# Kernel optimization log

Hardware: AMD Instinct MI355X
Metric: run time of the kernel (lower is better)

The kernel has to match this reference:

```python
import jax, jax.numpy as jnp
import numpy as np

D_MODEL = 64

def setup_inputs() -> dict:
    key = jax.random.key(0)
    k1, k2, k3, k4 = jax.random.split(key, 4)
    B, T, E = 4, 4096, 128
    x = jax.random.normal(k1, (B, T, E), dtype=jnp.float32)
    # nn.Linear weights, stored transposed as (in, out) for x @ W
    s = 1.0 / np.sqrt(E)
    Wq = jax.random.uniform(k2, (E, D_MODEL), jnp.float32, -s, s)
    Wk = jax.random.uniform(k3, (E, D_MODEL), jnp.float32, -s, s)
    Wv = jax.random.uniform(k4, (E, D_MODEL), jnp.float32, -s, s)
    return {"x": x, "Wq": Wq, "Wk": Wk, "Wv": Wv}

def reference(x, Wq, Wk, Wv):
    B, T, E = x.shape
    q = jnp.einsum('bte,ed->btd', x, Wq)
    k = jnp.einsum('bte,ed->btd', x, Wk)
    v = jnp.einsum('bte,ed->btd', x, Wv)
    scores = jnp.einsum('bqd,bkd->bqk', q, k) / np.sqrt(D_MODEL)  # [B,T,T]
    causal = jnp.tril(jnp.ones((T, T), dtype=bool))
    scores = jnp.where(causal, scores, jnp.float32(-1e9))
    attn = jax.nn.softmax(scores, axis=-1)
    # dropout p=0.0 -> identity (eval-mode faithful)
    return jnp.einsum('bqk,bkd->bqd', attn, v)
```

## Files before the change

kernel.cpp:

```cpp
#include <hip/hip_runtime.h>
#include <hip/hip_bf16.h>


typedef __attribute__((ext_vector_type(4))) float  f32x4;
typedef __attribute__((ext_vector_type(4))) unsigned int u32x4;
typedef __attribute__((ext_vector_type(8))) __bf16 bf16x8;
typedef __attribute__((ext_vector_type(8))) unsigned short u16x8;
typedef __attribute__((ext_vector_type(4))) unsigned short u16x4;

#define T_SEQ 4096
#define DH    64
#define EDIM  128
#define KVB   64
#define KSTR  72

__device__ __forceinline__ unsigned short f2bf(float f) {
    unsigned int x = __builtin_bit_cast(unsigned int, f);
    unsigned int r = x + 0x7fffu + ((x >> 16) & 1u);
    return (unsigned short)(r >> 16);
}

__device__ __forceinline__ unsigned int cvt_pk_bf16(float lo, float hi) {
    unsigned int d;
    asm("v_cvt_pk_bf16_f32 %0, %1, %2" : "=v"(d) : "v"(lo), "v"(hi));
    return d;
}

__device__ __forceinline__ f32x4 mfma_bf16(u16x8 a, u16x8 b, f32x4 c) {
    return __builtin_amdgcn_mfma_f32_16x16x32_bf16(
        __builtin_bit_cast(bf16x8, a), __builtin_bit_cast(bf16x8, b), c, 0, 0, 0);
}

__global__ __launch_bounds__(256) void prep_w_kernel(
    const float* __restrict__ wq, const float* __restrict__ wk,
    const float* __restrict__ wv, unsigned short* __restrict__ wt)
{
    int o = blockIdx.x * 256 + threadIdx.x;
    int m   = o >> 13;
    int rem = o & 8191;
    int d = rem >> 7, e = rem & 127;
    const float* W = (m == 0) ? wq : (m == 1) ? wk : wv;
    wt[o] = f2bf(W[e * DH + d]);
}

__global__ __launch_bounds__(64) void proj_kernel(
    const float* __restrict__ x, const unsigned short* __restrict__ wt,
    unsigned short* __restrict__ qw, unsigned short* __restrict__ kw,
    unsigned short* __restrict__ vt)
{
    const int l   = threadIdx.x;
    const int l15 = l & 15;
    const int lg  = l >> 4;
    const int row0 = blockIdx.x * 16;
    const int b    = row0 >> 12;
    const int t0   = row0 & 4095;

    u16x8 af[4];
    #pragma unroll
    for (int kt = 0; kt < 4; ++kt) {
        const float* xp = x + (row0 + l15) * EDIM + kt * 32 + lg * 8;
        f32x4 a = *(const f32x4*)xp;
        f32x4 bb = *(const f32x4*)(xp + 4);
        af[kt] = u16x8{ f2bf(a[0]), f2bf(a[1]), f2bf(a[2]), f2bf(a[3]),
                        f2bf(bb[0]), f2bf(bb[1]), f2bf(bb[2]), f2bf(bb[3]) };
    }

    unsigned short* outs[2] = { qw, kw };
    #pragma unroll
    for (int m = 0; m < 2; ++m) {
        #pragma unroll
        for (int nt = 0; nt < 4; ++nt) {
            f32x4 acc = {};
            #pragma unroll
            for (int kt = 0; kt < 4; ++kt) {
                u16x8 bfrag = *(const u16x8*)(wt + (m * 64 + nt * 16 + l15) * EDIM
                                                 + kt * 32 + lg * 8);
                acc = mfma_bf16(af[kt], bfrag, acc);
            }
            const float sc = (m == 0) ? 0.125f : 1.0f;
            #pragma unroll
            for (int r = 0; r < 4; ++r)
                outs[m][(row0 + lg * 4 + r) * DH + nt * 16 + l15] = f2bf(acc[r] * sc);
        }
    }

    #pragma unroll
    for (int nt = 0; nt < 4; ++nt) {
        f32x4 acc = {};
        #pragma unroll
        for (int kt = 0; kt < 4; ++kt) {
            u16x8 bfrag = *(const u16x8*)(wt + (2 * 64 + nt * 16 + l15) * EDIM
                                             + kt * 32 + lg * 8);
            acc = mfma_bf16(af[kt], bfrag, acc);
        }
        u16x4 pv = { f2bf(acc[0]), f2bf(acc[1]), f2bf(acc[2]), f2bf(acc[3]) };
        *(u16x4*)(vt + ((size_t)(b * DH + nt * 16 + l15)) * T_SEQ + t0 + lg * 4) = pv;
    }
}

struct St32s {
    f32x4 o[2][4];
    float m[2], l[2];
};

__device__ __forceinline__ void load_qf(
    const unsigned short* __restrict__ qg, int base, int qrow0,
    int l15, int lg, u16x8 qf[2][2])
{
    #pragma unroll
    for (int rt = 0; rt < 2; ++rt) {
        const unsigned short* qrow = qg + (base + qrow0 + rt * 16 + l15) * DH;
        qf[rt][0] = *(const u16x8*)(qrow + 0 + lg * 8);
        qf[rt][1] = *(const u16x8*)(qrow + 32 + lg * 8);
    }
}

__global__ __launch_bounds__(256, 4) void attn_partial_kernel(
    const unsigned short* __restrict__ qg, const unsigned short* __restrict__ kg,
    const unsigned short* __restrict__ vt,
    unsigned short* __restrict__ po, float* __restrict__ pm, float* __restrict__ pl)
{
    const int bid  = blockIdx.x;
    const int ch   = bid & 15;
    const int q128 = (bid >> 4) & 31;
    const int b    = bid >> 9;
    if (2 * ch > q128) return;

    __shared__ unsigned short K_lds[64 * KSTR];
    __shared__ unsigned short V_lds[64 * KSTR];

    const int tid = threadIdx.x;
    const int w   = tid >> 6;
    const int l   = tid & 63;
    const int l15 = l & 15;
    const int lg  = l >> 4;

    const int base   = b * T_SEQ;
    const int qrow0w = q128 * 128 + w * 32;
    const int kvb = ch * 256;
    const int kve = min(kvb + 256, q128 * 128 + 128);

    u16x8 qf[2][2];
    load_qf(qg, base, qrow0w, l15, lg, qf);

    St32s st;
    #pragma unroll
    for (int rt = 0; rt < 2; ++rt) {
        #pragma unroll
        for (int dt = 0; dt < 4; ++dt) st.o[rt][dt] = f32x4{};
        st.m[rt] = -1e30f; st.l[rt] = 0.0f;
    }

    const int src0 = l15 + 32 * (lg & 1);
    const int src1 = src0 + 16;
    const bool hi  = (lg >> 1) != 0;

    for (int kv0 = kvb; kv0 < kve; kv0 += KVB) {
        #pragma unroll
        for (int i = 0; i < 2; ++i) {
            int idx = tid + i * 256;
            int row = idx >> 3;
            int c8  = (idx & 7) * 8;
            *(u16x8*)&K_lds[row * KSTR + c8] =
                *(const u16x8*)(kg + (size_t)(base + kv0 + row) * DH + c8);
            *(u16x8*)&V_lds[row * KSTR + c8] =
                *(const u16x8*)(vt + (size_t)(b * DH + row) * T_SEQ + kv0 + c8);
        }
        __syncthreads();

        if (kv0 <= qrow0w + 31) {
            u16x8 kf[4][2];
            #pragma unroll
            for (int nt = 0; nt < 4; ++nt)
                #pragma unroll
                for (int kt = 0; kt < 2; ++kt)
                    kf[nt][kt] = *(const u16x8*)&K_lds[(nt * 16 + l15) * KSTR
                                                       + kt * 32 + lg * 8];

            f32x4 s[2][4];
            __builtin_amdgcn_s_setprio(1);
            #pragma unroll
            for (int rt = 0; rt < 2; ++rt)
                #pragma unroll
                for (int nt = 0; nt < 4; ++nt) {
                    f32x4 a = {};
                    a = mfma_bf16(kf[nt][0], qf[rt][0], a);
                    a = mfma_bf16(kf[nt][1], qf[rt][1], a);
                    s[rt][nt] = a;
                }
            __builtin_amdgcn_s_setprio(0);

            if (kv0 + KVB - 1 > qrow0w) {
                #pragma unroll
                for (int rt = 0; rt < 2; ++rt)
                    #pragma unroll
                    for (int nt = 0; nt < 4; ++nt)
                        #pragma unroll
                        for (int r = 0; r < 4; ++r) {
                            int kj = kv0 + nt * 16 + lg * 4 + r;
                            int qi = qrow0w + rt * 16 + l15;
                            if (kj > qi) s[rt][nt][r] = -1e30f;
                        }
            }

            float sc2[2];
            bool grow = false;
            unsigned int pk[2][4][2];
            #pragma unroll
            for (int rt = 0; rt < 2; ++rt) {
                float mx = s[rt][0][0];
                #pragma unroll
                for (int nt = 0; nt < 4; ++nt)
                    #pragma unroll
                    for (int r = 0; r < 4; ++r)
                        mx = fmaxf(mx, s[rt][nt][r]);
                mx = fmaxf(mx, __shfl_xor(mx, 16));
                mx = fmaxf(mx, __shfl_xor(mx, 32));

                float mold = st.m[rt];
                float mnew = fmaxf(mold, mx);
                grow |= (mx > mold);
                float sc = __expf(mold - mnew);
                sc2[rt] = sc;
                st.m[rt] = mnew;

                float rs = 0.0f;
                #pragma unroll
                for (int nt = 0; nt < 4; ++nt)
                    #pragma unroll
                    for (int r = 0; r < 4; ++r) {
                        float p = __expf(s[rt][nt][r] - mnew);
                        s[rt][nt][r] = p;
                        rs += p;
                    }
                rs += __shfl_xor(rs, 16);
                rs += __shfl_xor(rs, 32);
                st.l[rt] = st.l[rt] * sc + rs;

                #pragma unroll
                for (int nt = 0; nt < 4; ++nt) {
                    pk[rt][nt][0] = cvt_pk_bf16(s[rt][nt][0], s[rt][nt][1]);
                    pk[rt][nt][1] = cvt_pk_bf16(s[rt][nt][2], s[rt][nt][3]);
                }
            }
            if (__any(grow)) {
                #pragma unroll
                for (int rt = 0; rt < 2; ++rt)
                    #pragma unroll
                    for (int dt = 0; dt < 4; ++dt)
                        st.o[rt][dt] *= sc2[rt];
            }

            __builtin_amdgcn_s_setprio(1);
            #pragma unroll
            for (int kt = 0; kt < 2; ++kt) {
                u16x8 vf[4];
                #pragma unroll
                for (int dt = 0; dt < 4; ++dt)
                    vf[dt] = *(const u16x8*)&V_lds[(dt * 16 + l15) * KSTR
                                                   + kt * 32 + lg * 8];
                #pragma unroll
                for (int rt = 0; rt < 2; ++rt) {
                    unsigned int pb[4];
                    #pragma unroll
                    for (int t = 0; t < 4; ++t) {
                        int src = (t < 2) ? src0 : src1;
                        unsigned int pa  = __shfl(pk[rt][2 * kt][t & 1], src);
                        unsigned int pbv = __shfl(pk[rt][2 * kt + 1][t & 1], src);
                        pb[t] = hi ? pbv : pa;
                    }
                    u32x4 pbq = { pb[0], pb[1], pb[2], pb[3] };
                    u16x8 pbf = __builtin_bit_cast(u16x8, pbq);
                    #pragma unroll
                    for (int dt = 0; dt < 4; ++dt)
                        st.o[rt][dt] = mfma_bf16(vf[dt], pbf, st.o[rt][dt]);
                }
            }
            __builtin_amdgcn_s_setprio(0);
        }
        __syncthreads();
    }

    const int pidx = (b * 32 + q128) * 16 + ch;
    unsigned short* pob = po + (size_t)pidx * 8192;
    #pragma unroll
    for (int rt = 0; rt < 2; ++rt) {
        int row = w * 32 + rt * 16 + l15;
        #pragma unroll
        for (int dt = 0; dt < 4; ++dt) {
            unsigned int w0 = cvt_pk_bf16(st.o[rt][dt][0], st.o[rt][dt][1]);
            unsigned int w1 = cvt_pk_bf16(st.o[rt][dt][2], st.o[rt][dt][3]);
            *(unsigned int*)&pob[row * 64 + dt * 16 + lg * 4]     = w0;
            *(unsigned int*)&pob[row * 64 + dt * 16 + lg * 4 + 2] = w1;
        }
        if (lg == 0) {
            pm[pidx * 128 + row] = st.m[rt];
            pl[pidx * 128 + row] = st.l[rt];
        }
    }
}

__global__ __launch_bounds__(256) void attn_combine_kernel(
    const unsigned short* __restrict__ po, const float* __restrict__ pm,
    const float* __restrict__ pl, float* __restrict__ out)
{
    const int blk  = blockIdx.x;
    const int half = blk & 1;
    const int tb   = blk >> 1;
    const int q128 = tb & 31;
    const int b    = tb >> 5;
    const int nch  = (q128 >> 1) + 1;
    const int row  = half * 64 + (threadIdx.x >> 2);
    const int d0   = (threadIdx.x & 3) * 16;
    const int bp   = tb * 16;

    float mstar = -1e30f;
    for (int i = 0; i < nch; ++i)
        mstar = fmaxf(mstar, pm[(bp + i) * 128 + row]);

    float lsum = 0.0f;
    float a[16] = {};
    for (int i = 0; i < nch; ++i) {
        float wi = __expf(pm[(bp + i) * 128 + row] - mstar);
        lsum += wi * pl[(bp + i) * 128 + row];
        const unsigned short* p = po + (size_t)(bp + i) * 8192 + row * 64 + d0;
        u16x8 v0 = *(const u16x8*)p;
        u16x8 v1 = *(const u16x8*)(p + 8);
        #pragma unroll
        for (int j = 0; j < 8; ++j) {
            unsigned int u0 = (unsigned int)v0[j] << 16;
            unsigned int u1 = (unsigned int)v1[j] << 16;
            a[j]     += wi * __builtin_bit_cast(float, u0);
            a[8 + j] += wi * __builtin_bit_cast(float, u1);
        }
    }
    const float inv = 1.0f / lsum;
    float* op = out + (size_t)(b * T_SEQ + q128 * 128 + row) * DH + d0;
    #pragma unroll
    for (int j = 0; j < 4; ++j) {
        f32x4 o0 = { a[4*(j&1)+0 + 8*(j>>1)] * inv, a[4*(j&1)+1 + 8*(j>>1)] * inv,
                     a[4*(j&1)+2 + 8*(j>>1)] * inv, a[4*(j&1)+3 + 8*(j>>1)] * inv };
        *(f32x4*)(op + j * 4) = o0;
    }
}

__device__ __forceinline__ void flash32s_global(
    const unsigned short* __restrict__ kp,
    const unsigned short* __restrict__ vp,
    int qrow0, int kv_begin, int kv_end,
    const u16x8 qf[2][2], St32s& st, int l15, int lg)
{
    const int src0 = l15 + 32 * (lg & 1);
    const int src1 = src0 + 16;
    const bool hi  = (lg >> 1) != 0;

    for (int kv0 = kv_begin; kv0 < kv_end; kv0 += KVB) {
        u16x8 kf[4][2];
        #pragma unroll
        for (int nt = 0; nt < 4; ++nt)
            #pragma unroll
            for (int kt = 0; kt < 2; ++kt)
                kf[nt][kt] = *(const u16x8*)(kp + (kv0 + nt * 16 + l15) * DH
                                                + kt * 32 + lg * 8);

        f32x4 s[2][4];
        #pragma unroll
        for (int rt = 0; rt < 2; ++rt)
            #pragma unroll
            for (int nt = 0; nt < 4; ++nt) {
                f32x4 a = {};
                a = mfma_bf16(kf[nt][0], qf[rt][0], a);
                a = mfma_bf16(kf[nt][1], qf[rt][1], a);
                s[rt][nt] = a;
            }

        if (kv0 + KVB - 1 > qrow0) {
            #pragma unroll
            for (int rt = 0; rt < 2; ++rt)
                #pragma unroll
                for (int nt = 0; nt < 4; ++nt)
                    #pragma unroll
                    for (int r = 0; r < 4; ++r) {
                        int kj = kv0 + nt * 16 + lg * 4 + r;
                        int qi = qrow0 + rt * 16 + l15;
                        if (kj > qi) s[rt][nt][r] = -1e30f;
                    }
        }

        float sc2[2];
        bool grow = false;
        unsigned int pk[2][4][2];
        #pragma unroll
        for (int rt = 0; rt < 2; ++rt) {
            float mx = s[rt][0][0];
            #pragma unroll
            for (int nt = 0; nt < 4; ++nt)
                #pragma unroll
                for (int r = 0; r < 4; ++r)
                    mx = fmaxf(mx, s[rt][nt][r]);
            mx = fmaxf(mx, __shfl_xor(mx, 16));
            mx = fmaxf(mx, __shfl_xor(mx, 32));

            float mold = st.m[rt];
            float mnew = fmaxf(mold, mx);
            grow |= (mx > mold);
            float sc = __expf(mold - mnew);
            sc2[rt] = sc;
            st.m[rt] = mnew;

            float rs = 0.0f;
            #pragma unroll
            for (int nt = 0; nt < 4; ++nt)
                #pragma unroll
                for (int r = 0; r < 4; ++r) {
                    float p = __expf(s[rt][nt][r] - mnew);
                    s[rt][nt][r] = p;
                    rs += p;
                }
            rs += __shfl_xor(rs, 16);
            rs += __shfl_xor(rs, 32);
            st.l[rt] = st.l[rt] * sc + rs;

            #pragma unroll
            for (int nt = 0; nt < 4; ++nt) {
                pk[rt][nt][0] = cvt_pk_bf16(s[rt][nt][0], s[rt][nt][1]);
                pk[rt][nt][1] = cvt_pk_bf16(s[rt][nt][2], s[rt][nt][3]);
            }
        }
        if (__any(grow)) {
            #pragma unroll
            for (int rt = 0; rt < 2; ++rt)
                #pragma unroll
                for (int dt = 0; dt < 4; ++dt)
                    st.o[rt][dt] *= sc2[rt];
        }

        #pragma unroll
        for (int kt = 0; kt < 2; ++kt) {
            u16x8 vf[4];
            #pragma unroll
            for (int dt = 0; dt < 4; ++dt)
                vf[dt] = *(const u16x8*)(vp + (size_t)(dt * 16 + l15) * T_SEQ
                                            + kv0 + kt * 32 + lg * 8);
            #pragma unroll
            for (int rt = 0; rt < 2; ++rt) {
                unsigned int pb[4];
                #pragma unroll
                for (int t = 0; t < 4; ++t) {
                    int src = (t < 2) ? src0 : src1;
                    unsigned int pa  = __shfl(pk[rt][2 * kt][t & 1], src);
                    unsigned int pbv = __shfl(pk[rt][2 * kt + 1][t & 1], src);
                    pb[t] = hi ? pbv : pa;
                }
                u32x4 pbq = { pb[0], pb[1], pb[2], pb[3] };
                u16x8 pbf = __builtin_bit_cast(u16x8, pbq);
                #pragma unroll
                for (int dt = 0; dt < 4; ++dt)
                    st.o[rt][dt] = mfma_bf16(vf[dt], pbf, st.o[rt][dt]);
            }
        }
    }
}

__global__ __launch_bounds__(64, 4) void attn_direct_kernel(
    const unsigned short* __restrict__ qg, const unsigned short* __restrict__ kg,
    const unsigned short* __restrict__ vt, float* __restrict__ out)
{
    const int bid = blockIdx.x;
    const int q32 = bid & 127;
    const int b   = bid >> 7;
    const int l = threadIdx.x, l15 = l & 15, lg = l >> 4;
    const int qrow0 = q32 * 32;
    const int base  = b * T_SEQ;

    u16x8 qf[2][2];
    load_qf(qg, base, qrow0, l15, lg, qf);

    St32s st;
    #pragma unroll
    for (int rt = 0; rt < 2; ++rt) {
        #pragma unroll
        for (int dt = 0; dt < 4; ++dt) st.o[rt][dt] = f32x4{};
        st.m[rt] = -1e30f; st.l[rt] = 0.0f;
    }

    flash32s_global(kg + (size_t)base * DH, vt + (size_t)b * DH * T_SEQ,
                    qrow0, 0, qrow0 + 32, qf, st, l15, lg);

    #pragma unroll
    for (int rt = 0; rt < 2; ++rt) {
        float inv = 1.0f / st.l[rt];
        int row = base + qrow0 + rt * 16 + l15;
        #pragma unroll
        for (int dt = 0; dt < 4; ++dt) {
            f32x4 ov = st.o[rt][dt] * inv;
            *(f32x4*)&out[(size_t)row * DH + dt * 16 + lg * 4] = ov;
        }
    }
}

extern "C" void kernel_launch(void* const* d_in, const int* in_sizes, int n_in,
                              void* d_out, int out_size, void* d_ws, size_t ws_size,
                              hipStream_t stream)
{
    const float* x  = (const float*)d_in[0];
    const float* wq = (const float*)d_in[1];
    const float* wk = (const float*)d_in[2];
    const float* wv = (const float*)d_in[3];
    float* out = (float*)d_out;

    unsigned short* wt = (unsigned short*)d_ws;
    unsigned short* qw = (unsigned short*)((char*)d_ws + 65536);
    unsigned short* kw = qw + (size_t)16384 * DH;
    unsigned short* vt = kw + (size_t)16384 * DH;

    const size_t po_off = 65536u + 3u * 16384u * DH * 2u;
    const size_t po_sz  = (size_t)2048 * 128 * 64 * 2;
    const size_t pm_off = po_off + po_sz;
    const size_t pl_off = pm_off + (size_t)2048 * 128 * 4;
    const size_t need   = pl_off + (size_t)2048 * 128 * 4;

    prep_w_kernel<<<96, 256, 0, stream>>>(wq, wk, wv, wt);
    proj_kernel<<<1024, 64, 0, stream>>>(x, wt, qw, kw, vt);

    if (ws_size >= need) {
        unsigned short* po = (unsigned short*)((char*)d_ws + po_off);
        float* pm = (float*)((char*)d_ws + pm_off);
        float* pl = (float*)((char*)d_ws + pl_off);
        attn_partial_kernel<<<4 * 32 * 16, 256, 0, stream>>>(qw, kw, vt, po, pm, pl);
        attn_combine_kernel<<<4 * 32 * 2, 256, 0, stream>>>(po, pm, pl, out);
    } else {
        attn_direct_kernel<<<4 * 128, 64, 0, stream>>>(qw, kw, vt, out);
    }
}
```

Measured before the change: 69.90 us.

## Compact causal grid, prefetch second KV half into registers, use exp2 softmax

Replaces the 16-chunk grid that early-exits masked blocks with a compact triangular mapping of 272 live blocks per batch, decoded via sqrt. Each block stages 128 keys of K/V into larger LDS buffers at once and register-prefetches the second 128 while computing the first, cutting per-tile barriers and hiding global latency. Q is prescaled by log2(e)/8 so softmax and combine use exp2f instead of __expf. Larger LDS lowers the occupancy hint from 4 to 3 blocks, and more registers are held live for the prefetch.

After: 60.53 us. -13.4%, faster.

```diff
diff --git a/kernel.cpp b/kernel.cpp
--- a/kernel.cpp
+++ b/kernel.cpp
@@ -13,6 +13,8 @@
 #define EDIM  128
 #define KVB   64
 #define KSTR  72
+#define VSTR  136
+#define QSCALE 0.18033688f
 
 __device__ __forceinline__ unsigned short f2bf(float f) {
     unsigned int x = __builtin_bit_cast(unsigned int, f);
@@ -77,7 +79,7 @@
                                                  + kt * 32 + lg * 8);
                 acc = mfma_bf16(af[kt], bfrag, acc);
             }
-            const float sc = (m == 0) ? 0.125f : 1.0f;
+            const float sc = (m == 0) ? QSCALE : 1.0f;
             #pragma unroll
             for (int r = 0; r < 4; ++r)
                 outs[m][(row0 + lg * 4 + r) * DH + nt * 16 + l15] = f2bf(acc[r] * sc);
@@ -98,36 +100,57 @@
     }
 }
 
-struct St32s {
-    f32x4 o[2][4];
-    float m[2], l[2];
-};
-
-__device__ __forceinline__ void load_qf(
-    const unsigned short* __restrict__ qg, int base, int qrow0,
-    int l15, int lg, u16x8 qf[2][2])
-{
-    #pragma unroll
-    for (int rt = 0; rt < 2; ++rt) {
-        const unsigned short* qrow = qg + (base + qrow0 + rt * 16 + l15) * DH;
-        qf[rt][0] = *(const u16x8*)(qrow + 0 + lg * 8);
-        qf[rt][1] = *(const u16x8*)(qrow + 32 + lg * 8);
-    }
-}
-
-__global__ __launch_bounds__(256, 4) void attn_partial_kernel(
+__device__ __forceinline__ void loadK(u16x8 kr[4], const unsigned short* kgB,
+                                      int kv0, int tid) {
+    #pragma unroll
+    for (int j = 0; j < 4; ++j) {
+        int gi = tid + j * 256;
+        kr[j] = *(const u16x8*)(kgB + (size_t)(kv0 + (gi >> 3)) * DH + (gi & 7) * 8);
+    }
+}
+__device__ __forceinline__ void loadV(u16x8 vr[4], const unsigned short* vtB,
+                                      int kv0, int tid) {
+    #pragma unroll
+    for (int j = 0; j < 4; ++j) {
+        int gi = tid + j * 256;
+        vr[j] = *(const u16x8*)(vtB + (size_t)(gi >> 4) * T_SEQ + kv0 + (gi & 15) * 8);
+    }
+}
+__device__ __forceinline__ void writeK(const u16x8 kr[4], unsigned short* K_lds,
+                                       int tid) {
+    #pragma unroll
+    for (int j = 0; j < 4; ++j) {
+        int gi = tid + j * 256;
+        *(u16x8*)&K_lds[(gi >> 3) * KSTR + (gi & 7) * 8] = kr[j];
+    }
+}
+__device__ __forceinline__ void writeV(const u16x8 vr[4], unsigned short* V_lds,
+                                       int tid) {
+    #pragma unroll
+    for (int j = 0; j < 4; ++j) {
+        int gi = tid + j * 256;
+        *(u16x8*)&V_lds[(gi >> 4) * VSTR + (gi & 15) * 8] = vr[j];
+    }
+}
+
+__global__ __launch_bounds__(256, 3) void attn_partial_kernel(
     const unsigned short* __restrict__ qg, const unsigned short* __restrict__ kg,
     const unsigned short* __restrict__ vt,
     unsigned short* __restrict__ po, float* __restrict__ pm, float* __restrict__ pl)
 {
-    const int bid  = blockIdx.x;
-    const int ch   = bid & 15;
-    const int q128 = (bid >> 4) & 31;
-    const int b    = bid >> 9;
-    if (2 * ch > q128) return;
-
-    __shared__ unsigned short K_lds[64 * KSTR];
-    __shared__ unsigned short V_lds[64 * KSTR];
+    const int bid = blockIdx.x;
+    const int b   = bid / 272;
+    const int i   = bid - b * 272;
+    int k = (int)((__builtin_sqrtf((float)(4 * i + 1)) - 1.0f) * 0.5f);
+    while (k * (k + 1) > i) --k;
+    while ((k + 1) * (k + 2) <= i) ++k;
+    const int r    = i - k * (k + 1);
+    const int hiq  = (r >= k + 1);
+    const int q128 = 2 * k + hiq;
+    const int ch   = hiq ? r - (k + 1) : r;
+
+    __shared__ unsigned short K_lds[128 * KSTR];
+    __shared__ unsigned short V_lds[64 * VSTR];
 
     const int tid = threadIdx.x;
     const int w   = tid >> 6;
@@ -139,146 +162,166 @@
     const int qrow0w = q128 * 128 + w * 32;
     const int kvb = ch * 256;
     const int kve = min(kvb + 256, q128 * 128 + 128);
+    const bool ng2 = (kve - kvb) > 128;
+
+    const unsigned short* kgB = kg + (size_t)base * DH;
+    const unsigned short* vtB = vt + (size_t)b * DH * T_SEQ;
 
     u16x8 qf[2][2];
-    load_qf(qg, base, qrow0w, l15, lg, qf);
-
-    St32s st;
     #pragma unroll
     for (int rt = 0; rt < 2; ++rt) {
-        #pragma unroll
-        for (int dt = 0; dt < 4; ++dt) st.o[rt][dt] = f32x4{};
-        st.m[rt] = -1e30f; st.l[rt] = 0.0f;
+        const unsigned short* qrow = qg + (base + qrow0w + rt * 16 + l15) * DH;
+        qf[rt][0] = *(const u16x8*)(qrow + 0 + lg * 8);
+        qf[rt][1] = *(const u16x8*)(qrow + 32 + lg * 8);
+    }
+
+    f32x4 o_acc[2][4];
+    float m_run[2], l_run[2];
+    #pragma unroll
+    for (int rt = 0; rt < 2; ++rt) {
+        #pragma unroll
+        for (int dt = 0; dt < 4; ++dt) o_acc[rt][dt] = f32x4{};
+        m_run[rt] = -1e30f; l_run[rt] = 0.0f;
     }
 
     const int src0 = l15 + 32 * (lg & 1);
     const int src1 = src0 + 16;
     const bool hi  = (lg >> 1) != 0;
 
-    for (int kv0 = kvb; kv0 < kve; kv0 += KVB) {
-        #pragma unroll
-        for (int i = 0; i < 2; ++i) {
-            int idx = tid + i * 256;
-            int row = idx >> 3;
-            int c8  = (idx & 7) * 8;
-            *(u16x8*)&K_lds[row * KSTR + c8] =
-                *(const u16x8*)(kg + (size_t)(base + kv0 + row) * DH + c8);
-            *(u16x8*)&V_lds[row * KSTR + c8] =
-                *(const u16x8*)(vt + (size_t)(b * DH + row) * T_SEQ + kv0 + c8);
-        }
-        __syncthreads();
-
-        if (kv0 <= qrow0w + 31) {
-            u16x8 kf[4][2];
-            #pragma unroll
-            for (int nt = 0; nt < 4; ++nt)
-                #pragma unroll
-                for (int kt = 0; kt < 2; ++kt)
-                    kf[nt][kt] = *(const u16x8*)&K_lds[(nt * 16 + l15) * KSTR
-                                                       + kt * 32 + lg * 8];
-
-            f32x4 s[2][4];
-            __builtin_amdgcn_s_setprio(1);
+    auto compute_tile = [&](int kv0, int tt) {
+        if (kv0 > qrow0w + 31) return;
+        const unsigned short* Kt = K_lds + (tt * 64) * KSTR;
+        const unsigned short* Vt = V_lds + tt * 64;
+
+        u16x8 kf[4][2];
+        #pragma unroll
+        for (int nt = 0; nt < 4; ++nt)
+            #pragma unroll
+            for (int kt = 0; kt < 2; ++kt)
+                kf[nt][kt] = *(const u16x8*)&Kt[(nt * 16 + l15) * KSTR
+                                                + kt * 32 + lg * 8];
+
+        f32x4 s[2][4];
+        __builtin_amdgcn_s_setprio(1);
+        #pragma unroll
+        for (int rt = 0; rt < 2; ++rt)
+            #pragma unroll
+            for (int nt = 0; nt < 4; ++nt) {
+                f32x4 a = {};
+                a = mfma_bf16(kf[nt][0], qf[rt][0], a);
+                a = mfma_bf16(kf[nt][1], qf[rt][1], a);
+                s[rt][nt] = a;
+            }
+        __builtin_amdgcn_s_setprio(0);
+
+        if (kv0 + KVB - 1 > qrow0w) {
             #pragma unroll
             for (int rt = 0; rt < 2; ++rt)
-                #pragma unroll
-                for (int nt = 0; nt < 4; ++nt) {
-                    f32x4 a = {};
-                    a = mfma_bf16(kf[nt][0], qf[rt][0], a);
-                    a = mfma_bf16(kf[nt][1], qf[rt][1], a);
-                    s[rt][nt] = a;
-                }
-            __builtin_amdgcn_s_setprio(0);
-
-            if (kv0 + KVB - 1 > qrow0w) {
-                #pragma unroll
-                for (int rt = 0; rt < 2; ++rt)
-                    #pragma unroll
-                    for (int nt = 0; nt < 4; ++nt)
-                        #pragma unroll
-                        for (int r = 0; r < 4; ++r) {
-                            int kj = kv0 + nt * 16 + lg * 4 + r;
-                            int qi = qrow0w + rt * 16 + l15;
-                            if (kj > qi) s[rt][nt][r] = -1e30f;
-                        }
-            }
-
-            float sc2[2];
-            bool grow = false;
-            unsigned int pk[2][4][2];
-            #pragma unroll
-            for (int rt = 0; rt < 2; ++rt) {
-                float mx = s[rt][0][0];
                 #pragma unroll
                 for (int nt = 0; nt < 4; ++nt)
                     #pragma unroll
-                    for (int r = 0; r < 4; ++r)
-                        mx = fmaxf(mx, s[rt][nt][r]);
-                mx = fmaxf(mx, __shfl_xor(mx, 16));
-                mx = fmaxf(mx, __shfl_xor(mx, 32));
-
-                float mold = st.m[rt];
-                float mnew = fmaxf(mold, mx);
-                grow |= (mx > mold);
-                float sc = __expf(mold - mnew);
-                sc2[rt] = sc;
-                st.m[rt] = mnew;
-
-                float rs = 0.0f;
-                #pragma unroll
-                for (int nt = 0; nt < 4; ++nt)
-                    #pragma unroll
-                    for (int r = 0; r < 4; ++r) {
-                        float p = __expf(s[rt][nt][r] - mnew);
-                        s[rt][nt][r] = p;
-                        rs += p;
+                    for (int rr = 0; rr < 4; ++rr) {
+                        int kj = kv0 + nt * 16 + lg * 4 + rr;
+                        int qi = qrow0w + rt * 16 + l15;
+                        if (kj > qi) s[rt][nt][rr] = -1e30f;
                     }
-                rs += __shfl_xor(rs, 16);
-                rs += __shfl_xor(rs, 32);
-                st.l[rt] = st.l[rt] * sc + rs;
-
-                #pragma unroll
-                for (int nt = 0; nt < 4; ++nt) {
-                    pk[rt][nt][0] = cvt_pk_bf16(s[rt][nt][0], s[rt][nt][1]);
-                    pk[rt][nt][1] = cvt_pk_bf16(s[rt][nt][2], s[rt][nt][3]);
+        }
+
+        float sc2[2];
+        bool grow = false;
+        unsigned int pk[2][4][2];
+        #pragma unroll
+        for (int rt = 0; rt < 2; ++rt) {
+            float mx = s[rt][0][0];
+            #pragma unroll
+            for (int nt = 0; nt < 4; ++nt)
+                #pragma unroll
+                for (int rr = 0; rr < 4; ++rr)
+                    mx = fmaxf(mx, s[rt][nt][rr]);
+            mx = fmaxf(mx, __shfl_xor(mx, 16));
+            mx = fmaxf(mx, __shfl_xor(mx, 32));
+
+            float mold = m_run[rt];
+            float mnew = fmaxf(mold, mx);
+            grow |= (mx > mold);
+            float sc = exp2f(mold - mnew);
+            sc2[rt] = sc;
+            m_run[rt] = mnew;
+
+            float rs = 0.0f;
+            #pragma unroll
+            for (int nt = 0; nt < 4; ++nt)
+                #pragma unroll
+                for (int rr = 0; rr < 4; ++rr) {
+                    float p = exp2f(s[rt][nt][rr] - mnew);
+                    s[rt][nt][rr] = p;
+                    rs += p;
                 }
-            }
-            if (__any(grow)) {
-                #pragma unroll
-                for (int rt = 0; rt < 2; ++rt)
-                    #pragma unroll
-                    for (int dt = 0; dt < 4; ++dt)
-                        st.o[rt][dt] *= sc2[rt];
-            }
-
-            __builtin_amdgcn_s_setprio(1);
-            #pragma unroll
-            for (int kt = 0; kt < 2; ++kt) {
-                u16x8 vf[4];
+            rs += __shfl_xor(rs, 16);
+            rs += __shfl_xor(rs, 32);
+            l_run[rt] = l_run[rt] * sc + rs;
+
+            #pragma unroll
+            for (int nt = 0; nt < 4; ++nt) {
+                pk[rt][nt][0] = cvt_pk_bf16(s[rt][nt][0], s[rt][nt][1]);
+                pk[rt][nt][1] = cvt_pk_bf16(s[rt][nt][2], s[rt][nt][3]);
+            }
+        }
+        if (__any(grow)) {
+            #pragma unroll
+            for (int rt = 0; rt < 2; ++rt)
                 #pragma unroll
                 for (int dt = 0; dt < 4; ++dt)
-                    vf[dt] = *(const u16x8*)&V_lds[(dt * 16 + l15) * KSTR
-                                                   + kt * 32 + lg * 8];
-                #pragma unroll
-                for (int rt = 0; rt < 2; ++rt) {
-                    unsigned int pb[4];
-                    #pragma unroll
-                    for (int t = 0; t < 4; ++t) {
-                        int src = (t < 2) ? src0 : src1;
-                        unsigned int pa  = __shfl(pk[rt][2 * kt][t & 1], src);
-                        unsigned int pbv = __shfl(pk[rt][2 * kt + 1][t & 1], src);
-                        pb[t] = hi ? pbv : pa;
-                    }
-                    u32x4 pbq = { pb[0], pb[1], pb[2], pb[3] };
-                    u16x8 pbf = __builtin_bit_cast(u16x8, pbq);
-                    #pragma unroll
-                    for (int dt = 0; dt < 4; ++dt)
-                        st.o[rt][dt] = mfma_bf16(vf[dt], pbf, st.o[rt][dt]);
+                    o_acc[rt][dt] *= sc2[rt];
+        }
+
+        __builtin_amdgcn_s_setprio(1);
+        #pragma unroll
+        for (int kt = 0; kt < 2; ++kt) {
+            u16x8 vf[4];
+            #pragma unroll
+            for (int dt = 0; dt < 4; ++dt)
+                vf[dt] = *(const u16x8*)&Vt[(dt * 16 + l15) * VSTR
+                                            + kt * 32 + lg * 8];
+            #pragma unroll
+            for (int rt = 0; rt < 2; ++rt) {
+                unsigned int pb[4];
+                #pragma unroll
+                for (int t = 0; t < 4; ++t) {
+                    int src = (t < 2) ? src0 : src1;
+                    unsigned int pa  = __shfl(pk[rt][2 * kt][t & 1], src);
+                    unsigned int pbv = __shfl(pk[rt][2 * kt + 1][t & 1], src);
+                    pb[t] = hi ? pbv : pa;
                 }
-            }
-            __builtin_amdgcn_s_setprio(0);
-        }
+                u32x4 pbq = { pb[0], pb[1], pb[2], pb[3] };
+                u16x8 pbf = __builtin_bit_cast(u16x8, pbq);
+                #pragma unroll
+                for (int dt = 0; dt < 4; ++dt)
+                    o_acc[rt][dt] = mfma_bf16(vf[dt], pbf, o_acc[rt][dt]);
+            }
+        }
+        __builtin_amdgcn_s_setprio(0);
+    };
+
+    u16x8 kr[4], vr[4];
+    loadK(kr, kgB, kvb, tid);
+    loadV(vr, vtB, kvb, tid);
+    writeK(kr, K_lds, tid);
+    writeV(vr, V_lds, tid);
+    __syncthreads();
+
+    if (ng2) loadK(kr, kgB, kvb + 128, tid);
+    compute_tile(kvb, 0);
+    if (ng2) loadV(vr, vtB, kvb + 128, tid);
+    compute_tile(kvb + 64, 1);
+    __syncthreads();
+
+    if (ng2) {
+        writeK(kr, K_lds, tid);
+        writeV(vr, V_lds, tid);
         __syncthreads();
+        compute_tile(kvb + 128, 0);
+        compute_tile(kvb + 192, 1);
     }
 
     const int pidx = (b * 32 + q128) * 16 + ch;
@@ -288,14 +331,14 @@
         int row = w * 32 + rt * 16 + l15;
         #pragma unroll
         for (int dt = 0; dt < 4; ++dt) {
-            unsigned int w0 = cvt_pk_bf16(st.o[rt][dt][0], st.o[rt][dt][1]);
-            unsigned int w1 = cvt_pk_bf16(st.o[rt][dt][2], st.o[rt][dt][3]);
+            unsigned int w0 = cvt_pk_bf16(o_acc[rt][dt][0], o_acc[rt][dt][1]);
+            unsigned int w1 = cvt_pk_bf16(o_acc[rt][dt][2], o_acc[rt][dt][3]);
             *(unsigned int*)&pob[row * 64 + dt * 16 + lg * 4]     = w0;
             *(unsigned int*)&pob[row * 64 + dt * 16 + lg * 4 + 2] = w1;
         }
         if (lg == 0) {
-            pm[pidx * 128 + row] = st.m[rt];
-            pl[pidx * 128 + row] = st.l[rt];
+            pm[pidx * 128 + row] = m_run[rt];
+            pl[pidx * 128 + row] = l_run[rt];
         }
     }
 }
@@ -321,7 +364,7 @@
     float lsum = 0.0f;
     float a[16] = {};
     for (int i = 0; i < nch; ++i) {
-        float wi = __expf(pm[(bp + i) * 128 + row] - mstar);
+        float wi = exp2f(pm[(bp + i) * 128 + row] - mstar);
         lsum += wi * pl[(bp + i) * 128 + row];
         const unsigned short* p = po + (size_t)(bp + i) * 8192 + row * 64 + d0;
         u16x8 v0 = *(const u16x8*)p;
@@ -341,124 +384,6 @@
         f32x4 o0 = { a[4*(j&1)+0 + 8*(j>>1)] * inv, a[4*(j&1)+1 + 8*(j>>1)] * inv,
                      a[4*(j&1)+2 + 8*(j>>1)] * inv, a[4*(j&1)+3 + 8*(j>>1)] * inv };
         *(f32x4*)(op + j * 4) = o0;
-    }
-}
-
-__device__ __forceinline__ void flash32s_global(
-    const unsigned short* __restrict__ kp,
-    const unsigned short* __restrict__ vp,
-    int qrow0, int kv_begin, int kv_end,
-    const u16x8 qf[2][2], St32s& st, int l15, int lg)
-{
-    const int src0 = l15 + 32 * (lg & 1);
-    const int src1 = src0 + 16;
-    const bool hi  = (lg >> 1) != 0;
-
-    for (int kv0 = kv_begin; kv0 < kv_end; kv0 += KVB) {
-        u16x8 kf[4][2];
-        #pragma unroll
-        for (int nt = 0; nt < 4; ++nt)
-            #pragma unroll
-            for (int kt = 0; kt < 2; ++kt)
-                kf[nt][kt] = *(const u16x8*)(kp + (kv0 + nt * 16 + l15) * DH
-                                                + kt * 32 + lg * 8);
-
-        f32x4 s[2][4];
-        #pragma unroll
-        for (int rt = 0; rt < 2; ++rt)
-            #pragma unroll
-            for (int nt = 0; nt < 4; ++nt) {
-                f32x4 a = {};
-                a = mfma_bf16(kf[nt][0], qf[rt][0], a);
-                a = mfma_bf16(kf[nt][1], qf[rt][1], a);
-                s[rt][nt] = a;
-            }
-
-        if (kv0 + KVB - 1 > qrow0) {
-            #pragma unroll
-            for (int rt = 0; rt < 2; ++rt)
-                #pragma unroll
-                for (int nt = 0; nt < 4; ++nt)
-                    #pragma unroll
-                    for (int r = 0; r < 4; ++r) {
-                        int kj = kv0 + nt * 16 + lg * 4 + r;
-                        int qi = qrow0 + rt * 16 + l15;
-                        if (kj > qi) s[rt][nt][r] = -1e30f;
-                    }
-        }
-
-        float sc2[2];
-        bool grow = false;
-        unsigned int pk[2][4][2];
-        #pragma unroll
-        for (int rt = 0; rt < 2; ++rt) {
-            float mx = s[rt][0][0];
-            #pragma unroll
-            for (int nt = 0; nt < 4; ++nt)
-                #pragma unroll
-                for (int r = 0; r < 4; ++r)
-                    mx = fmaxf(mx, s[rt][nt][r]);
-            mx = fmaxf(mx, __shfl_xor(mx, 16));
-            mx = fmaxf(mx, __shfl_xor(mx, 32));
-
-            float mold = st.m[rt];
-            float mnew = fmaxf(mold, mx);
-            grow |= (mx > mold);
-            float sc = __expf(mold - mnew);
-            sc2[rt] = sc;
-            st.m[rt] = mnew;
-
-            float rs = 0.0f;
-            #pragma unroll
-            for (int nt = 0; nt < 4; ++nt)
-                #pragma unroll
-                for (int r = 0; r < 4; ++r) {
-                    float p = __expf(s[rt][nt][r] - mnew);
-                    s[rt][nt][r] = p;
-                    rs += p;
-                }
-            rs += __shfl_xor(rs, 16);
-            rs += __shfl_xor(rs, 32);
-            st.l[rt] = st.l[rt] * sc + rs;
-
-            #pragma unroll
-            for (int nt = 0; nt < 4; ++nt) {
-                pk[rt][nt][0] = cvt_pk_bf16(s[rt][nt][0], s[rt][nt][1]);
-                pk[rt][nt][1] = cvt_pk_bf16(s[rt][nt][2], s[rt][nt][3]);
-            }
-        }
-        if (__any(grow)) {
-            #pragma unroll
-            for (int rt = 0; rt < 2; ++rt)
-                #pragma unroll
-                for (int dt = 0; dt < 4; ++dt)
-                    st.o[rt][dt] *= sc2[rt];
-        }
-
-        #pragma unroll
-        for (int kt = 0; kt < 2; ++kt) {
-            u16x8 vf[4];
-            #pragma unroll
-            for (int dt = 0; dt < 4; ++dt)
-                vf[dt] = *(const u16x8*)(vp + (size_t)(dt * 16 + l15) * T_SEQ
-                                            + kv0 + kt * 32 + lg * 8);
-            #pragma unroll
-            for (int rt = 0; rt < 2; ++rt) {
-                unsigned int pb[4];
-                #pragma unroll
-                for (int t = 0; t < 4; ++t) {
-                    int src = (t < 2) ? src0 : src1;
-                    unsigned int pa  = __shfl(pk[rt][2 * kt][t & 1], src);
-                    unsigned int pbv = __shfl(pk[rt][2 * kt + 1][t & 1], src);
-                    pb[t] = hi ? pbv : pa;
-                }
-                u32x4 pbq = { pb[0], pb[1], pb[2], pb[3] };
-                u16x8 pbf = __builtin_bit_cast(u16x8, pbq);
-                #pragma unroll
-                for (int dt = 0; dt < 4; ++dt)
-                    st.o[rt][dt] = mfma_bf16(vf[dt], pbf, st.o[rt][dt]);
-            }
-        }
     }
 }
 
@@ -472,28 +397,137 @@
     const int l = threadIdx.x, l15 = l & 15, lg = l >> 4;
     const int qrow0 = q32 * 32;
     const int base  = b * T_SEQ;
+    const unsigned short* kp = kg + (size_t)base * DH;
+    const unsigned short* vp = vt + (size_t)b * DH * T_SEQ;
 
     u16x8 qf[2][2];
-    load_qf(qg, base, qrow0, l15, lg, qf);
-
-    St32s st;
     #pragma unroll
     for (int rt = 0; rt < 2; ++rt) {
-        #pragma unroll
-        for (int dt = 0; dt < 4; ++dt) st.o[rt][dt] = f32x4{};
-        st.m[rt] = -1e30f; st.l[rt] = 0.0f;
-    }
-
-    flash32s_global(kg + (size_t)base * DH, vt + (size_t)b * DH * T_SEQ,
-                    qrow0, 0, qrow0 + 32, qf, st, l15, lg);
-
+        const unsigned short* qrow = qg + (base + qrow0 + rt * 16 + l15) * DH;
+        qf[rt][0] = *(const u16x8*)(qrow + 0 + lg * 8);
+        qf[rt][1] = *(const u16x8*)(qrow + 32 + lg * 8);
+    }
+
+    f32x4 o_acc[2][4];
+    float m_run[2], l_run[2];
     #pragma unroll
     for (int rt = 0; rt < 2; ++rt) {
-        float inv = 1.0f / st.l[rt];
+        #pragma unroll
+        for (int dt = 0; dt < 4; ++dt) o_acc[rt][dt] = f32x4{};
+        m_run[rt] = -1e30f; l_run[rt] = 0.0f;
+    }
+
+    const int src0 = l15 + 32 * (lg & 1);
+    const int src1 = src0 + 16;
+    const bool hi  = (lg >> 1) != 0;
+
+    for (int kv0 = 0; kv0 <= qrow0 + 31; kv0 += KVB) {
+        u16x8 kf[4][2];
+        #pragma unroll
+        for (int nt = 0; nt < 4; ++nt)
+            #pragma unroll
+            for (int kt = 0; kt < 2; ++kt)
+                kf[nt][kt] = *(const u16x8*)(kp + (kv0 + nt * 16 + l15) * DH
+                                                + kt * 32 + lg * 8);
+        f32x4 s[2][4];
+        #pragma unroll
+        for (int rt = 0; rt < 2; ++rt)
+            #pragma unroll
+            for (int nt = 0; nt < 4; ++nt) {
+                f32x4 a = {};
+                a = mfma_bf16(kf[nt][0], qf[rt][0], a);
+                a = mfma_bf16(kf[nt][1], qf[rt][1], a);
+                s[rt][nt] = a;
+            }
+        if (kv0 + KVB - 1 > qrow0) {
+            #pragma unroll
+            for (int rt = 0; rt < 2; ++rt)
+                #pragma unroll
+                for (int nt = 0; nt < 4; ++nt)
+                    #pragma unroll
+                    for (int rr = 0; rr < 4; ++rr) {
+                        int kj = kv0 + nt * 16 + lg * 4 + rr;
+                        int qi = qrow0 + rt * 16 + l15;
+                        if (kj > qi) s[rt][nt][rr] = -1e30f;
+                    }
+        }
+        float sc2[2];
+        bool grow = false;
+        unsigned int pk[2][4][2];
+        #pragma unroll
+        for (int rt = 0; rt < 2; ++rt) {
+            float mx = s[rt][0][0];
+            #pragma unroll
+            for (int nt = 0; nt < 4; ++nt)
+                #pragma unroll
+                for (int rr = 0; rr < 4; ++rr)
+                    mx = fmaxf(mx, s[rt][nt][rr]);
+            mx = fmaxf(mx, __shfl_xor(mx, 16));
+            mx = fmaxf(mx, __shfl_xor(mx, 32));
+            float mold = m_run[rt];
+            float mnew = fmaxf(mold, mx);
+            grow |= (mx > mold);
+            float sc = exp2f(mold - mnew);
+            sc2[rt] = sc;
+            m_run[rt] = mnew;
+            float rs = 0.0f;
+            #pragma unroll
+            for (int nt = 0; nt < 4; ++nt)
+                #pragma unroll
+                for (int rr = 0; rr < 4; ++rr) {
+                    float p = exp2f(s[rt][nt][rr] - mnew);
+                    s[rt][nt][rr] = p;
+                    rs += p;
+                }
+            rs += __shfl_xor(rs, 16);
+            rs += __shfl_xor(rs, 32);
+            l_run[rt] = l_run[rt] * sc + rs;
+            #pragma unroll
+            for (int nt = 0; nt < 4; ++nt) {
+                pk[rt][nt][0] = cvt_pk_bf16(s[rt][nt][0], s[rt][nt][1]);
+                pk[rt][nt][1] = cvt_pk_bf16(s[rt][nt][2], s[rt][nt][3]);
+            }
+        }
+        if (__any(grow)) {
+            #pragma unroll
+            for (int rt = 0; rt < 2; ++rt)
+                #pragma unroll
+                for (int dt = 0; dt < 4; ++dt)
+                    o_acc[rt][dt] *= sc2[rt];
+        }
+        #pragma unroll
+        for (int kt = 0; kt < 2; ++kt) {
+            u16x8 vf[4];
+            #pragma unroll
+            for (int dt = 0; dt < 4; ++dt)
+                vf[dt] = *(const u16x8*)(vp + (size_t)(dt * 16 + l15) * T_SEQ
+                                            + kv0 + kt * 32 + lg * 8);
+            #pragma unroll
+            for (int rt = 0; rt < 2; ++rt) {
+                unsigned int pb[4];
+                #pragma unroll
+                for (int t = 0; t < 4; ++t) {
+                    int src = (t < 2) ? src0 : src1;
+                    unsigned int pa  = __shfl(pk[rt][2 * kt][t & 1], src);
+                    unsigned int pbv = __shfl(pk[rt][2 * kt + 1][t & 1], src);
+                    pb[t] = hi ? pbv : pa;
+                }
+                u32x4 pbq = { pb[0], pb[1], pb[2], pb[3] };
+                u16x8 pbf = __builtin_bit_cast(u16x8, pbq);
+                #pragma unroll
+                for (int dt = 0; dt < 4; ++dt)
+                    o_acc[rt][dt] = mfma_bf16(vf[dt], pbf, o_acc[rt][dt]);
+            }
+        }
+    }
+
+    #pragma unroll
+    for (int rt = 0; rt < 2; ++rt) {
+        float inv = 1.0f / l_run[rt];
         int row = base + qrow0 + rt * 16 + l15;
         #pragma unroll
         for (int dt = 0; dt < 4; ++dt) {
-            f32x4 ov = st.o[rt][dt] * inv;
+            f32x4 ov = o_acc[rt][dt] * inv;
             *(f32x4*)&out[(size_t)row * DH + dt * 16 + lg * 4] = ov;
         }
     }
@@ -527,7 +561,7 @@
         unsigned short* po = (unsigned short*)((char*)d_ws + po_off);
         float* pm = (float*)((char*)d_ws + pm_off);
         float* pl = (float*)((char*)d_ws + pl_off);
-        attn_partial_kernel<<<4 * 32 * 16, 256, 0, stream>>>(qw, kw, vt, po, pm, pl);
+        attn_partial_kernel<<<4 * 272, 256, 0, stream>>>(qw, kw, vt, po, pm, pl);
         attn_combine_kernel<<<4 * 32 * 2, 256, 0, stream>>>(po, pm, pl, out);
     } else {
         attn_direct_kernel<<<4 * 128, 64, 0, stream>>>(qw, kw, vt, out);
```
